# Kernel optimization log

Hardware: AMD Instinct MI355X
Metric: run time of the kernel (lower is better)

## Reference

```python
import jax, jax.numpy as jnp
import numpy as np

N_NODES = 100000
N_EDGES = 3200000
NEG_SLOPE = 0.2  # PyG GATConv default leaky_relu slope


def gat_layer(x, src, dst, W, att_src, att_dst, bias, heads, out_ch, concat):
    N = x.shape[0]
    h = (x @ W).reshape(N, heads, out_ch)              # [N, H, C]
    a_src = jnp.sum(h * att_src[None], axis=-1)        # [N, H]
    a_dst = jnp.sum(h * att_dst[None], axis=-1)        # [N, H]
    e = jax.nn.leaky_relu(a_src[src] + a_dst[dst], NEG_SLOPE)  # [E, H]
    m = jax.ops.segment_max(e, dst, num_segments=N)    # segment softmax (stable)
    e = jnp.exp(e - m[dst])
    s = jax.ops.segment_sum(e, dst, num_segments=N)
    alpha = e / (s[dst] + 1e-16)                       # [E, H]
    msg = h[src] * alpha[:, :, None]                   # [E, H, C]
    out = jax.ops.segment_sum(msg, dst, num_segments=N)  # [N, H, C]
    out = out.reshape(N, heads * out_ch) if concat else out.mean(axis=1)
    return out + bias


def setup_inputs() -> dict:
    key = jax.random.key(0)
    ks = jax.random.split(key, 8)
    x = jax.random.normal(ks[0], (N_NODES, 512), dtype=jnp.float32)
    edge_index = jax.random.randint(ks[1], (2, N_EDGES), 0, N_NODES, dtype=jnp.int64)
    s1 = 1.0 / np.sqrt(512.0)
    s2 = 1.0 / np.sqrt(64.0)
    return {
        "x": x,
        "edge_index": edge_index,
        "W1": jax.random.normal(ks[2], (512, 64), dtype=jnp.float32) * s1,
        "att_src1": jax.random.normal(ks[3], (8, 8), dtype=jnp.float32) * s2,
        "att_dst1": jax.random.normal(ks[4], (8, 8), dtype=jnp.float32) * s2,
        "b1": jnp.zeros((64,), dtype=jnp.float32),
        "W2": jax.random.normal(ks[5], (64, 16), dtype=jnp.float32) * s2,
        "att_src2": jax.random.normal(ks[6], (1, 16), dtype=jnp.float32) * 0.25,
        "att_dst2": jax.random.normal(ks[7], (1, 16), dtype=jnp.float32) * 0.25,
        "b2": jnp.zeros((16,), dtype=jnp.float32),
    }


def reference(x, edge_index, W1, att_src1, att_dst1, b1, W2, att_src2, att_dst2, b2):
    N = x.shape[0]
    # add self-loops (PyG GATConv default) so every node has at least one edge
    loops = jnp.arange(N, dtype=edge_index.dtype)
    src = jnp.concatenate([edge_index[0], loops])
    dst = jnp.concatenate([edge_index[1], loops])
    # eval mode: dropout(p=0.6, training=False) is identity
    h = jax.nn.elu(gat_layer(x, src, dst, W1, att_src1, att_dst1, b1, 8, 8, True))
    z = gat_layer(h, src, dst, W2, att_src2, att_dst2, b2, 1, 16, False)
    return jax.nn.log_softmax(z, axis=1)
```

## Files before the change

### kernel.cpp

```cpp
#include <hip/hip_runtime.h>
#include <hip/hip_bf16.h>
#include <math.h>

#define LEAKY 0.2f
#define BSHIFT 7
#define NBUCK_MAX 1024
#define BCAP 6144
#define CHUNK 8192
#define CCAP 6656

typedef __attribute__((ext_vector_type(8))) short short8v;
typedef __attribute__((ext_vector_type(4))) float f32x4;

__device__ __forceinline__ unsigned pkbf(float a, float b) {
  __hip_bfloat162 t = __float22bfloat162_rn(make_float2(a, b));
  return *(unsigned*)&t;
}
__device__ __forceinline__ unsigned short f2bf(float f) {
  __hip_bfloat16 h = __float2bfloat16(f);
  return *(unsigned short*)&h;
}
__device__ __forceinline__ float bflo(unsigned u) { return __uint_as_float(u << 16); }
__device__ __forceinline__ float bfhi(unsigned u) { return __uint_as_float(u & 0xFFFF0000u); }

__global__ __launch_bounds__(256) void setup_kernel(
    const float* __restrict__ W1, unsigned short* __restrict__ w1t,
    int* __restrict__ bucketCursor) {
  int t = blockIdx.x * 256 + threadIdx.x;
  if (t < 64 * 512) {
    int k = t & 511, c = t >> 9;
    w1t[(size_t)c * 512 + k] = f2bf(W1[(size_t)k * 64 + c]);
  }
  if (t < NBUCK_MAX) bucketCursor[t] = t * BCAP;
}

__global__ __launch_bounds__(256) void binB_kernel(
    const int* __restrict__ src, const int* __restrict__ dst,
    int* __restrict__ bucketCursor, unsigned* __restrict__ ebuf,
    int E, int Etot, int NBUCK) {
  __shared__ unsigned stage[CHUNK];
  __shared__ unsigned short sbk[CHUNK];
  __shared__ int bcnt[NBUCK_MAX];
  __shared__ int bres[NBUCK_MAX];
  __shared__ int bcur[NBUCK_MAX];
  const int t = threadIdx.x;
  const int c0 = blockIdx.x * CHUNK;
  const int cnt = min(CHUNK, Etot - c0);
  for (int i = t; i < NBUCK_MAX; i += 256) bcnt[i] = 0;
  __syncthreads();
  for (int i = t; i < cnt; i += 256) {
    int g = c0 + i;
    int s, d;
    if (g < E) { s = src[g]; d = dst[g]; } else { s = d = g - E; }
    stage[i] = (unsigned)s | ((unsigned)(d & 127) << 20);
    sbk[i] = (unsigned short)(d >> BSHIFT);
    atomicAdd(&bcnt[d >> BSHIFT], 1);
  }
  __syncthreads();
  for (int i = t; i < NBUCK; i += 256) {
    int c = bcnt[i];
    bres[i] = c ? atomicAdd(&bucketCursor[i], c) : 0;
    bcur[i] = 0;
  }
  __syncthreads();
  for (int i = t; i < cnt; i += 256) {
    int b = sbk[i];
    int slot = bres[b] + atomicAdd(&bcur[b], 1);
    ebuf[slot] = stage[i];
  }
}

__global__ __launch_bounds__(256) void binC_kernel(
    const unsigned* __restrict__ ebuf, const int* __restrict__ bucketCursor,
    int2* __restrict__ seg, int* __restrict__ esrc, int N) {
  __shared__ unsigned stage[CCAP];
  __shared__ int hist[128];
  __shared__ int sA[128];
  __shared__ int curs[128];
  const int t = threadIdx.x;
  const int b = blockIdx.x;
  const int lo = b * BCAP;
  const int cnt = bucketCursor[b] - lo;
  const int base = b << BSHIFT;
  if (t < 128) hist[t] = 0;
  __syncthreads();
  for (int i = t; i < cnt; i += 256) {
    unsigned p = ebuf[lo + i];
    stage[i] = p;
    atomicAdd(&hist[p >> 20], 1);
  }
  __syncthreads();
  int v = 0;
  if (t < 128) { v = hist[t]; sA[t] = v; }
  __syncthreads();
  for (int off = 1; off < 128; off <<= 1) {
    int u = 0;
    if (t < 128 && t >= off) u = sA[t - off];
    __syncthreads();
    if (t < 128) sA[t] += u;
    __syncthreads();
  }
  if (t < 128) {
    int excl = sA[t] - v;
    curs[t] = excl;
    if (base + t < N) seg[base + t] = make_int2(lo + excl, v);
  }
  __syncthreads();
  for (int i = t; i < cnt; i += 256) {
    unsigned p = stage[i];
    int pos = atomicAdd(&curs[p >> 20], 1);
    esrc[lo + pos] = (int)(p & 0xFFFFFu);
  }
}

__global__ __launch_bounds__(256) void gemm1_kernel(
    const float* __restrict__ x, const unsigned short* __restrict__ w1t,
    unsigned short* __restrict__ h1b, int M) {
  __shared__ __align__(16) unsigned short AsU[128][40];
  __shared__ __align__(16) unsigned short BtU[64][40];
  const int tid = threadIdx.x;
  const int m0 = blockIdx.x * 128;
  const int w = tid >> 6, lane = tid & 63;
  const int l15 = lane & 15, lhi = lane >> 4;

  f32x4 acc[2][4];
#pragma unroll
  for (int r = 0; r < 2; ++r)
#pragma unroll
    for (int t = 0; t < 4; ++t) acc[r][t] = (f32x4){0.f, 0.f, 0.f, 0.f};

  float4 pv[4];
  short8v pw;
  const int cB = tid >> 2, kbB = (tid & 3) * 8;

#pragma unroll
  for (int u = 0; u < 4; ++u) {
    int q = u * 256 + tid;
    int r = q >> 3, c4 = q & 7;
    int gm = m0 + r;
    pv[u] = (gm < M) ? *(const float4*)(x + (size_t)gm * 512 + c4 * 4)
                     : make_float4(0.f, 0.f, 0.f, 0.f);
  }
  pw = *(const short8v*)(w1t + (size_t)cB * 512 + kbB);

  for (int k0 = 0; k0 < 512; k0 += 32) {
#pragma unroll
    for (int u = 0; u < 4; ++u) {
      int q = u * 256 + tid;
      int r = q >> 3, c4 = q & 7;
      *(uint2*)&AsU[r][c4 * 4] =
          make_uint2(pkbf(pv[u].x, pv[u].y), pkbf(pv[u].z, pv[u].w));
    }
    *(short8v*)&BtU[cB][kbB] = pw;
    __syncthreads();

    if (k0 + 32 < 512) {
      int k1 = k0 + 32;
#pragma unroll
      for (int u = 0; u < 4; ++u) {
        int q = u * 256 + tid;
        int r = q >> 3, c4 = q & 7;
        int gm = m0 + r;
        pv[u] = (gm < M) ? *(const float4*)(x + (size_t)gm * 512 + k1 + c4 * 4)
                         : make_float4(0.f, 0.f, 0.f, 0.f);
      }
      pw = *(const short8v*)(w1t + (size_t)cB * 512 + k1 + kbB);
    }

    short8v a0 = *(const short8v*)&AsU[32 * w + l15][lhi * 8];
    short8v a1 = *(const short8v*)&AsU[32 * w + 16 + l15][lhi * 8];
#pragma unroll
    for (int t = 0; t < 4; ++t) {
      short8v b = *(const short8v*)&BtU[16 * t + l15][lhi * 8];
      acc[0][t] = __builtin_amdgcn_mfma_f32_16x16x32_bf16(a0, b, acc[0][t], 0, 0, 0);
      acc[1][t] = __builtin_amdgcn_mfma_f32_16x16x32_bf16(a1, b, acc[1][t], 0, 0, 0);
    }
    __syncthreads();
  }
#pragma unroll
  for (int rt = 0; rt < 2; ++rt) {
#pragma unroll
    for (int t = 0; t < 4; ++t) {
#pragma unroll
      for (int reg = 0; reg < 4; ++reg) {
        int gm = m0 + 32 * w + 16 * rt + 4 * lhi + reg;
        if (gm < M) h1b[(size_t)gm * 64 + 16 * t + l15] = f2bf(acc[rt][t][reg]);
      }
    }
  }
}

__global__ __launch_bounds__(256) void agg1_kernel(
    const int2* __restrict__ seg, const int* __restrict__ esrc,
    const unsigned short* __restrict__ h1b, const float* __restrict__ att_src,
    const float* __restrict__ att_dst, const float* __restrict__ b1,
    const float* __restrict__ W2, unsigned short* __restrict__ g2b, int N) {
  __shared__ float Ws[1024];
  {
    float4 v = ((const float4*)W2)[threadIdx.x & 255];
    *(float4*)&Ws[(threadIdx.x & 255) * 4] = v;
  }
  __syncthreads();
  int wid = (blockIdx.x * 256 + threadIdx.x) >> 6;
  int lane = threadIdx.x & 63;
  if (wid >= N) return;
  const int n = wid;
  const int eo = lane >> 3, q = lane & 7;
  float as[8], ad[8];
  {
    float4 t0 = *(const float4*)(att_src + 8 * q);
    float4 t1 = *(const float4*)(att_src + 8 * q + 4);
    as[0] = t0.x; as[1] = t0.y; as[2] = t0.z; as[3] = t0.w;
    as[4] = t1.x; as[5] = t1.y; as[6] = t1.z; as[7] = t1.w;
    t0 = *(const float4*)(att_dst + 8 * q);
    t1 = *(const float4*)(att_dst + 8 * q + 4);
    ad[0] = t0.x; ad[1] = t0.y; ad[2] = t0.z; ad[3] = t0.w;
    ad[4] = t1.x; ad[5] = t1.y; ad[6] = t1.z; ad[7] = t1.w;
  }
  float adn;
  {
    uint4 hv = *(const uint4*)(h1b + (size_t)n * 64 + 8 * q);
    adn = bflo(hv.x) * ad[0] + bfhi(hv.x) * ad[1] + bflo(hv.y) * ad[2] +
          bfhi(hv.y) * ad[3] + bflo(hv.z) * ad[4] + bfhi(hv.z) * ad[5] +
          bflo(hv.w) * ad[6] + bfhi(hv.w) * ad[7];
  }
  const int2 sg = seg[n];
  const int s0 = sg.x, s1 = sg.x + sg.y;
  float acc[8] = {0.f, 0.f, 0.f, 0.f, 0.f, 0.f, 0.f, 0.f};
  float psum = 0.f;
  for (int i = s0 + eo; i < s1; i += 8) {
    int s = esrc[i];
    uint4 hv = *(const uint4*)(h1b + (size_t)s * 64 + 8 * q);
    float g[8];
    g[0] = bflo(hv.x); g[1] = bfhi(hv.x); g[2] = bflo(hv.y); g[3] = bfhi(hv.y);
    g[4] = bflo(hv.z); g[5] = bfhi(hv.z); g[6] = bflo(hv.w); g[7] = bfhi(hv.w);
    float u = g[0] * as[0] + g[1] * as[1] + g[2] * as[2] + g[3] * as[3] +
              g[4] * as[4] + g[5] * as[5] + g[6] * as[6] + g[7] * as[7];
    float e = u + adn;
    e = e > 0.f ? e : LEAKY * e;
    float p = __expf(e);
#pragma unroll
    for (int j = 0; j < 8; ++j) acc[j] += p * g[j];
    psum += p;
  }
#pragma unroll
  for (int off = 8; off <= 32; off <<= 1) {
#pragma unroll
    for (int j = 0; j < 8; ++j) acc[j] += __shfl_xor(acc[j], off);
    psum += __shfl_xor(psum, off);
  }
  float inv = 1.0f / (psum + 1e-16f);
  float4 b0 = *(const float4*)(b1 + 8 * q);
  float4 b14 = *(const float4*)(b1 + 8 * q + 4);
  float bb[8] = {b0.x, b0.y, b0.z, b0.w, b14.x, b14.y, b14.z, b14.w};
  float o[8];
#pragma unroll
  for (int j = 0; j < 8; ++j) {
    float v = acc[j] * inv + bb[j];
    o[j] = v > 0.f ? v : expm1f(v);
  }
  float p0 = 0.f, p1 = 0.f;
#pragma unroll
  for (int j = 0; j < 8; ++j) {
    float2 wv = *(const float2*)&Ws[(8 * q + j) * 16 + 2 * eo];
    p0 += o[j] * wv.x;
    p1 += o[j] * wv.y;
  }
  p0 += __shfl_xor(p0, 1); p0 += __shfl_xor(p0, 2); p0 += __shfl_xor(p0, 4);
  p1 += __shfl_xor(p1, 1); p1 += __shfl_xor(p1, 2); p1 += __shfl_xor(p1, 4);
  if (q == 0)
    *(unsigned*)&g2b[(size_t)n * 16 + 2 * eo] = pkbf(p0, p1);
}

__global__ __launch_bounds__(256) void agg2_kernel(
    const int2* __restrict__ seg, const int* __restrict__ esrc,
    const unsigned short* __restrict__ g2b, const float* __restrict__ att_src,
    const float* __restrict__ att_dst, const float* __restrict__ b2,
    float* __restrict__ out, int N) {
  int wid = (blockIdx.x * 256 + threadIdx.x) >> 6;
  int lane = threadIdx.x & 63;
  if (wid >= N) return;
  const int n = wid;
  const int eo = lane >> 2, q = lane & 3;
  const float4 as4 = *(const float4*)(att_src + 4 * q);
  const float4 ad4 = *(const float4*)(att_dst + 4 * q);

  float adn;
  {
    uint2 gv = *(const uint2*)(g2b + (size_t)n * 16 + 4 * q);
    float un = bflo(gv.x) * ad4.x + bfhi(gv.x) * ad4.y +
               bflo(gv.y) * ad4.z + bfhi(gv.y) * ad4.w;
    un += __shfl_xor(un, 1);
    un += __shfl_xor(un, 2);
    adn = un;
  }

  const int2 sg = seg[n];
  const int s0 = sg.x, s1 = sg.x + sg.y;
  float a0 = 0.f, a1 = 0.f, a2 = 0.f, a3 = 0.f, psum = 0.f;
  for (int i = s0 + eo; i < s1; i += 16) {
    int s = esrc[i];
    uint2 gv = *(const uint2*)(g2b + (size_t)s * 16 + 4 * q);
    float g0 = bflo(gv.x), g1 = bfhi(gv.x), g2v = bflo(gv.y), g3 = bfhi(gv.y);
    float u = g0 * as4.x + g1 * as4.y + g2v * as4.z + g3 * as4.w;
    u += __shfl_xor(u, 1);
    u += __shfl_xor(u, 2);
    float e = u + adn;
    e = e > 0.f ? e : LEAKY * e;
    float p = __expf(e);
    a0 += p * g0; a1 += p * g1; a2 += p * g2v; a3 += p * g3;
    psum += p;
  }
#pragma unroll
  for (int off = 4; off <= 32; off <<= 1) {
    a0 += __shfl_xor(a0, off);
    a1 += __shfl_xor(a1, off);
    a2 += __shfl_xor(a2, off);
    a3 += __shfl_xor(a3, off);
    psum += __shfl_xor(psum, off);
  }

  float inv = 1.0f / (psum + 1e-16f);
  float z0 = a0 * inv + b2[4 * q + 0];
  float z1 = a1 * inv + b2[4 * q + 1];
  float z2 = a2 * inv + b2[4 * q + 2];
  float z3 = a3 * inv + b2[4 * q + 3];
  float mx = fmaxf(fmaxf(z0, z1), fmaxf(z2, z3));
  mx = fmaxf(mx, __shfl_xor(mx, 1));
  mx = fmaxf(mx, __shfl_xor(mx, 2));
  float ex = __expf(z0 - mx) + __expf(z1 - mx) + __expf(z2 - mx) + __expf(z3 - mx);
  ex += __shfl_xor(ex, 1);
  ex += __shfl_xor(ex, 2);
  float lse = mx + logf(ex);
  if (eo == 0)
    *(float4*)(out + (size_t)n * 16 + 4 * q) =
        make_float4(z0 - lse, z1 - lse, z2 - lse, z3 - lse);
}

extern "C" void kernel_launch(void* const* d_in, const int* in_sizes, int n_in,
                              void* d_out, int out_size, void* d_ws, size_t ws_size,
                              hipStream_t stream) {
  const float* x        = (const float*)d_in[0];
  const int*   ei       = (const int*)d_in[1];
  const float* W1       = (const float*)d_in[2];
  const float* att_src1 = (const float*)d_in[3];
  const float* att_dst1 = (const float*)d_in[4];
  const float* b1       = (const float*)d_in[5];
  const float* W2       = (const float*)d_in[6];
  const float* att_src2 = (const float*)d_in[7];
  const float* att_dst2 = (const float*)d_in[8];
  const float* b2       = (const float*)d_in[9];
  float* out = (float*)d_out;

  const int N = in_sizes[0] / 512;
  const int E = in_sizes[1] / 2;
  const int Etot = E + N;
  const int NBUCK = (N + 127) >> BSHIFT;

  char* base = (char*)d_ws;
  size_t off = 0;
  auto alloc = [&](size_t bytes) { void* p = base + off; off = (off + bytes + 15) & ~(size_t)15; return p; };
  unsigned short* h1b = (unsigned short*)alloc((size_t)N * 64 * 2);
  unsigned short* g2b = (unsigned short*)alloc((size_t)N * 16 * 2);
  int*      esrc  = (int*)alloc((size_t)NBUCK * BCAP * 4);
  unsigned* ebuf  = (unsigned*)alloc((size_t)NBUCK * BCAP * 4);
  int2*     seg   = (int2*)alloc((size_t)N * 8);
  int* bucketCursor = (int*)alloc(NBUCK_MAX * 4);
  unsigned short* w1t = (unsigned short*)alloc(64 * 512 * 2);

  const int* srcI = ei;
  const int* dstI = ei + E;

  setup_kernel<<<128, 256, 0, stream>>>(W1, w1t, bucketCursor);
  binB_kernel<<<(Etot + CHUNK - 1) / CHUNK, 256, 0, stream>>>(
      srcI, dstI, bucketCursor, ebuf, E, Etot, NBUCK);
  binC_kernel<<<NBUCK, 256, 0, stream>>>(ebuf, bucketCursor, seg, esrc, N);

  gemm1_kernel<<<(N + 127) / 128, 256, 0, stream>>>(x, w1t, h1b, N);
  agg1_kernel<<<(N * 64 + 255) / 256, 256, 0, stream>>>(
      seg, esrc, h1b, att_src1, att_dst1, b1, W2, g2b, N);

  agg2_kernel<<<(N * 64 + 255) / 256, 256, 0, stream>>>(
      seg, esrc, g2b, att_src2, att_dst2, b2, out, N);
}
```

Before: 259.2 us.

## Merge bucket sort and GEMM into one launch; prefetch neighbor rows in aggregation

The second binning pass (binC) and the first-layer GEMM now run as one launch. The first NBUCK blocks do the CSR finalisation and the remaining blocks do the GEMM, sharing dynamically sized LDS. This lets the two independent stages overlap on the GPU and removes one launch boundary. Both aggregation loops also software-prefetch the next edge's source index and feature row, hiding gather latency at the cost of extra registers. The larger LDS allocation for GEMM blocks may lower occupancy.

```diff
diff --git a/kernel.cpp b/kernel.cpp
--- a/kernel.cpp
+++ b/kernel.cpp
@@ -8,6 +8,7 @@
 #define BCAP 6144
 #define CHUNK 8192
 #define CCAP 6656
+#define PHASE2_LDS 28160
 
 typedef __attribute__((ext_vector_type(8))) short short8v;
 typedef __attribute__((ext_vector_type(4))) float f32x4;
@@ -70,15 +71,15 @@
   }
 }
 
-__global__ __launch_bounds__(256) void binC_kernel(
-    const unsigned* __restrict__ ebuf, const int* __restrict__ bucketCursor,
-    int2* __restrict__ seg, int* __restrict__ esrc, int N) {
-  __shared__ unsigned stage[CCAP];
-  __shared__ int hist[128];
-  __shared__ int sA[128];
-  __shared__ int curs[128];
+__device__ __forceinline__ void binC_body(
+    char* smem, const unsigned* __restrict__ ebuf,
+    const int* __restrict__ bucketCursor, int2* __restrict__ seg,
+    int* __restrict__ esrc, int N, int b) {
+  unsigned* stage = (unsigned*)smem;
+  int* hist = (int*)(smem + CCAP * 4);
+  int* sA   = hist + 128;
+  int* curs = sA + 128;
   const int t = threadIdx.x;
-  const int b = blockIdx.x;
   const int lo = b * BCAP;
   const int cnt = bucketCursor[b] - lo;
   const int base = b << BSHIFT;
@@ -113,13 +114,15 @@
   }
 }
 
-__global__ __launch_bounds__(256) void gemm1_kernel(
-    const float* __restrict__ x, const unsigned short* __restrict__ w1t,
-    unsigned short* __restrict__ h1b, int M) {
-  __shared__ __align__(16) unsigned short AsU[128][40];
-  __shared__ __align__(16) unsigned short BtU[64][40];
+__device__ __forceinline__ void gemm1_body(
+    char* smem, const float* __restrict__ x,
+    const unsigned short* __restrict__ w1t, unsigned short* __restrict__ h1b,
+    int M, int blk) {
+  typedef unsigned short AsRow[40];
+  AsRow* AsU = (AsRow*)smem;
+  AsRow* BtU = (AsRow*)(smem + 128 * 40 * 2);
   const int tid = threadIdx.x;
-  const int m0 = blockIdx.x * 128;
+  const int m0 = blk * 128;
   const int w = tid >> 6, lane = tid & 63;
   const int l15 = lane & 15, lhi = lane >> 4;
 
@@ -187,6 +190,20 @@
         if (gm < M) h1b[(size_t)gm * 64 + 16 * t + l15] = f2bf(acc[rt][t][reg]);
       }
     }
+  }
+}
+
+__global__ __launch_bounds__(256) void phase2_kernel(
+    const unsigned* __restrict__ ebuf, const int* __restrict__ bucketCursor,
+    int2* __restrict__ seg, int* __restrict__ esrc, int N, int NBUCK,
+    const float* __restrict__ x, const unsigned short* __restrict__ w1t,
+    unsigned short* __restrict__ h1b) {
+  extern __shared__ __align__(16) char smem[];
+  const int b = blockIdx.x;
+  if (b < NBUCK) {
+    binC_body(smem, ebuf, bucketCursor, seg, esrc, N, b);
+  } else {
+    gemm1_body(smem, x, w1t, h1b, N, b - NBUCK);
   }
 }
 
@@ -228,9 +245,19 @@
   const int s0 = sg.x, s1 = sg.x + sg.y;
   float acc[8] = {0.f, 0.f, 0.f, 0.f, 0.f, 0.f, 0.f, 0.f};
   float psum = 0.f;
-  for (int i = s0 + eo; i < s1; i += 8) {
+  int i = s0 + eo;
+  uint4 hv;
+  if (i < s1) {
     int s = esrc[i];
-    uint4 hv = *(const uint4*)(h1b + (size_t)s * 64 + 8 * q);
+    hv = *(const uint4*)(h1b + (size_t)s * 64 + 8 * q);
+  }
+  for (; i < s1; ) {
+    const int i2 = i + 8;
+    uint4 hv_n;
+    if (i2 < s1) {
+      int s2 = esrc[i2];
+      hv_n = *(const uint4*)(h1b + (size_t)s2 * 64 + 8 * q);
+    }
     float g[8];
     g[0] = bflo(hv.x); g[1] = bfhi(hv.x); g[2] = bflo(hv.y); g[3] = bfhi(hv.y);
     g[4] = bflo(hv.z); g[5] = bfhi(hv.z); g[6] = bflo(hv.w); g[7] = bfhi(hv.w);
@@ -242,6 +269,8 @@
 #pragma unroll
     for (int j = 0; j < 8; ++j) acc[j] += p * g[j];
     psum += p;
+    hv = hv_n;
+    i = i2;
   }
 #pragma unroll
   for (int off = 8; off <= 32; off <<= 1) {
@@ -298,9 +327,19 @@
   const int2 sg = seg[n];
   const int s0 = sg.x, s1 = sg.x + sg.y;
   float a0 = 0.f, a1 = 0.f, a2 = 0.f, a3 = 0.f, psum = 0.f;
-  for (int i = s0 + eo; i < s1; i += 16) {
+  int i = s0 + eo;
+  uint2 gv;
+  if (i < s1) {
     int s = esrc[i];
-    uint2 gv = *(const uint2*)(g2b + (size_t)s * 16 + 4 * q);
+    gv = *(const uint2*)(g2b + (size_t)s * 16 + 4 * q);
+  }
+  for (; i < s1; ) {
+    const int i2 = i + 16;
+    uint2 gv_n;
+    if (i2 < s1) {
+      int s2 = esrc[i2];
+      gv_n = *(const uint2*)(g2b + (size_t)s2 * 16 + 4 * q);
+    }
     float g0 = bflo(gv.x), g1 = bfhi(gv.x), g2v = bflo(gv.y), g3 = bfhi(gv.y);
     float u = g0 * as4.x + g1 * as4.y + g2v * as4.z + g3 * as4.w;
     u += __shfl_xor(u, 1);
@@ -310,6 +349,8 @@
     float p = __expf(e);
     a0 += p * g0; a1 += p * g1; a2 += p * g2v; a3 += p * g3;
     psum += p;
+    gv = gv_n;
+    i = i2;
   }
 #pragma unroll
   for (int off = 4; off <= 32; off <<= 1) {
@@ -356,6 +397,7 @@
   const int E = in_sizes[1] / 2;
   const int Etot = E + N;
   const int NBUCK = (N + 127) >> BSHIFT;
+  const int GBLK = (N + 127) / 128;
 
   char* base = (char*)d_ws;
   size_t off = 0;
@@ -374,9 +416,10 @@
   setup_kernel<<<128, 256, 0, stream>>>(W1, w1t, bucketCursor);
   binB_kernel<<<(Etot + CHUNK - 1) / CHUNK, 256, 0, stream>>>(
       srcI, dstI, bucketCursor, ebuf, E, Etot, NBUCK);
-  binC_kernel<<<NBUCK, 256, 0, stream>>>(ebuf, bucketCursor, seg, esrc, N);
-
-  gemm1_kernel<<<(N + 127) / 128, 256, 0, stream>>>(x, w1t, h1b, N);
+
+  phase2_kernel<<<NBUCK + GBLK, 256, PHASE2_LDS, stream>>>(
+      ebuf, bucketCursor, seg, esrc, N, NBUCK, x, w1t, h1b);
+
   agg1_kernel<<<(N * 64 + 255) / 256, 256, 0, stream>>>(
       seg, esrc, h1b, att_src1, att_dst1, b1, W2, g2b, N);
 
```

Result: faster. 244.0 us, median of 2 (-5.8%).
